# Performance work log

Measured on AMD Instinct MI355X. Metric: run time of the kernel, lower is better.

Reference implementation:

```python
import jax, jax.numpy as jnp
import numpy as np

D_MODEL = 1024
NHEAD = 16
HEAD_DIM = D_MODEL // NHEAD
B, T = 2, 2048


def setup_inputs() -> dict:
    key = jax.random.key(0)
    ks = jax.random.split(key, 12)
    s = 1.0 / np.sqrt(D_MODEL)
    return {
        "query": jax.random.normal(ks[0], (B, T, D_MODEL), jnp.float32),
        "key": jax.random.normal(ks[1], (B, T, D_MODEL), jnp.float32),
        "value": jax.random.normal(ks[2], (B, T, D_MODEL), jnp.float32),
        "key_padding_mask": jnp.zeros((B, T), dtype=bool),
        "attn_mask": jnp.zeros((T, T), jnp.float32),
        "stoich_frac": jax.random.uniform(ks[3], (B, T), jnp.float32),
        "Wq": jax.random.uniform(ks[4], (D_MODEL, D_MODEL), jnp.float32, -s, s),
        "bq": jnp.zeros((D_MODEL,), jnp.float32),
        "Wk": jax.random.uniform(ks[5], (D_MODEL, D_MODEL), jnp.float32, -s, s),
        "bk": jnp.zeros((D_MODEL,), jnp.float32),
        "Wv": jax.random.uniform(ks[6], (D_MODEL, D_MODEL), jnp.float32, -s, s),
        "bv": jnp.zeros((D_MODEL,), jnp.float32),
        "Wo": jax.random.uniform(ks[7], (D_MODEL, D_MODEL), jnp.float32, -s, s),
        "bo": jnp.zeros((D_MODEL,), jnp.float32),
        "stoich_alpha": jnp.float32(0.1),
    }


def reference(query, key, value, key_padding_mask, attn_mask, stoich_frac,
              Wq, bq, Wk, bk, Wv, bv, Wo, bo, stoich_alpha):
    Bq, Tq, _ = query.shape
    Tk = key.shape[1]
    scale = HEAD_DIM ** -0.5
    # Linear projections (torch Linear: x @ W.T + b), reshape to [B, H, T, Dh]
    Q = (query @ Wq.T + bq).reshape(Bq, Tq, NHEAD, HEAD_DIM).transpose(0, 2, 1, 3)
    K = (key @ Wk.T + bk).reshape(Bq, Tk, NHEAD, HEAD_DIM).transpose(0, 2, 1, 3)
    V = (value @ Wv.T + bv).reshape(Bq, Tk, NHEAD, HEAD_DIM).transpose(0, 2, 1, 3)
    # Scores [B, H, Tq, Tk]
    scores = jnp.einsum("bhqd,bhkd->bhqk", Q, K) * scale
    # Stoichiometric pairwise bias (T_q == T_k path)
    diff = stoich_frac[:, :, None] - stoich_frac[:, None, :]  # [B, Tq, Tk]
    bias = stoich_alpha * (jnp.log1p(jnp.abs(diff)) * jnp.sign(diff))
    scores = scores + bias[:, None, :, :]
    scores = scores + attn_mask  # broadcasts [Tq, Tk]
    scores = jnp.where(key_padding_mask[:, None, None, :], -jnp.inf, scores)
    probs = jax.nn.softmax(scores, axis=-1)
    # dropout: eval mode / p=0 -> identity
    out = jnp.einsum("bhqk,bhkd->bhqd", probs, V)
    out = out.transpose(0, 2, 1, 3).reshape(Bq, Tq, D_MODEL)
    return out @ Wo.T + bo
```

## Files before the change

### kernel.cpp

```cpp
#include <hip/hip_runtime.h>
#include <math.h>

typedef __bf16 bf16_t;
typedef __bf16 bf16x8 __attribute__((ext_vector_type(8)));
typedef __bf16 bf16x4 __attribute__((ext_vector_type(4)));
typedef float  f32x4  __attribute__((ext_vector_type(4)));

#define NHEAD 16
#define HDIM 64
#define DMODEL 1024
#define TSEQ 2048
#define WEL (DMODEL * DMODEL)

#define SBAR() __builtin_amdgcn_s_barrier()
#define SCHED0() __builtin_amdgcn_sched_barrier(0)
#define LGKM0() do { asm volatile("s_waitcnt lgkmcnt(0)" ::: "memory"); \
                     __builtin_amdgcn_sched_barrier(0); } while (0)

__device__ __forceinline__ f32x4 mfma16(bf16x8 a, bf16x8 b, f32x4 c) {
  return __builtin_amdgcn_mfma_f32_16x16x32_bf16(a, b, c, 0, 0, 0);
}

__device__ __forceinline__ void gload16(const bf16_t* g, bf16_t* l) {
  __builtin_amdgcn_global_load_lds((const __attribute__((address_space(1))) void*)g,
                                   (__attribute__((address_space(3))) void*)l, 16, 0, 0);
}

__device__ __forceinline__ unsigned pk2(float lo, float hi) {
  unsigned short a = __builtin_bit_cast(unsigned short, (__bf16)lo);
  unsigned short c = __builtin_bit_cast(unsigned short, (__bf16)hi);
  return ((unsigned)c << 16) | a;
}

__device__ __forceinline__ void cvtstore(f32x4 x0, f32x4 x1, bf16_t* dh, bf16_t* dl, int off) {
  bf16x8 hfr, lfr;
#pragma unroll
  for (int j = 0; j < 4; ++j) {
    float v = x0[j];
    __bf16 hb = (__bf16)v;
    hfr[j] = hb; lfr[j] = (__bf16)(v - (float)hb);
    float w = x1[j];
    __bf16 wb = (__bf16)w;
    hfr[4 + j] = wb; lfr[4 + j] = (__bf16)(w - (float)wb);
  }
  *(bf16x8*)(dh + off) = hfr;
  *(bf16x8*)(dl + off) = lfr;
}

__global__ __launch_bounds__(256)
void presplit_w(const float* __restrict__ w0, const float* __restrict__ w1,
                const float* __restrict__ w2, const float* __restrict__ w3,
                bf16_t* __restrict__ out) {
  const int y = blockIdx.y;
  const float* src = (y == 0) ? w0 : (y == 1) ? w1 : (y == 2) ? w2 : w3;
  size_t i = ((size_t)blockIdx.x * 256 + threadIdx.x) * 8;
  f32x4 a = *(const f32x4*)(src + i);
  f32x4 c = *(const f32x4*)(src + i + 4);
  bf16x8 h, l;
#pragma unroll
  for (int j = 0; j < 4; ++j) {
    __bf16 hb = (__bf16)a[j];
    h[j] = hb; l[j] = (__bf16)(a[j] - (float)hb);
    __bf16 cb = (__bf16)c[j];
    h[4 + j] = cb; l[4 + j] = (__bf16)(c[j] - (float)cb);
  }
  bf16_t* dh = out + (size_t)y * 2 * WEL;
  *(bf16x8*)(dh + i) = h;
  *(bf16x8*)(dh + WEL + i) = l;
}

__global__ __launch_bounds__(256)
void build_bias(const float* __restrict__ amask, const unsigned char* __restrict__ kpm,
                const float* __restrict__ sf, const float* __restrict__ alpha_p,
                bf16_t* __restrict__ BM) {
  size_t idx = (size_t)blockIdx.x * 256 + threadIdx.x;
  int k8 = (int)(idx & (TSEQ / 8 - 1));
  size_t bq = idx >> 8;
  int b = (int)(bq >> 11);
  int q = (int)(bq & (TSEQ - 1));
  const float sfq = sf[bq];
  const float alpha = *alpha_p;
  const float* sfk = sf + (size_t)b * TSEQ + k8 * 8;
  const float* am  = amask + (size_t)q * TSEQ + k8 * 8;
  const unsigned char* kp = kpm + (size_t)b * TSEQ + k8 * 8;
  bf16x8 o;
#pragma unroll
  for (int j = 0; j < 8; ++j) {
    float df = sfq - sfk[j];
    float v = alpha * copysignf(log1pf(fabsf(df)), df) + am[j];
    if (kp[j]) v = -1.0e30f;
    o[j] = (__bf16)v;
  }
  *(bf16x8*)&BM[idx * 8] = o;
}

template<int MODE>
__global__ __launch_bounds__(512)
void gemm_qkv(const float* __restrict__ A, const bf16_t* __restrict__ Wh,
              const bf16_t* __restrict__ Wl, const float* __restrict__ bias,
              bf16_t* __restrict__ obh, bf16_t* __restrict__ obl) {
  __shared__ bf16_t AH[8 * 512], AL[8 * 512], WHs[2][4 * 512], WLs[2][4 * 512];
  const int tid = threadIdx.x;
  const int lane = tid & 63;
  const int a15 = lane & 15, g = lane >> 4;
  const int wv = tid >> 6, wm = wv >> 1, wn = wv & 1;
  const int m0 = blockIdx.y * 128, n0 = blockIdx.x * 64;
  f32x4 acc[2][2] = {};

  const int t0 = tid >> 6, l0 = tid & 63;
  const float* pA = A + (size_t)(m0 + t0 * 16 + (l0 & 15)) * DMODEL + 8 * (l0 >> 4);
  const int wts = wv & 3;
  const bf16_t* pWg = ((wv < 4) ? Wh : Wl) + (size_t)(n0 + wts * 16 + a15) * DMODEL + 8 * g;

  f32x4 rAa = *(const f32x4*)pA, rAb = *(const f32x4*)(pA + 4);
  gload16(pWg, (wv < 4) ? &WHs[0][wts * 512] : &WLs[0][wts * 512]);

  constexpr int NK = DMODEL / 32;
  for (int t = 0; t < NK; ++t) {
    const int cur = t & 1;
    SBAR();
    cvtstore(rAa, rAb, AH, AL, tid * 8);
    SCHED0();
    if (t + 1 < NK) {
      pA += 32;
      rAa = *(const f32x4*)pA; rAb = *(const f32x4*)(pA + 4);
      SCHED0();
      gload16(pWg + (t + 1) * 32, (wv < 4) ? &WHs[cur ^ 1][wts * 512]
                                           : &WLs[cur ^ 1][wts * 512]);
      SCHED0();
      asm volatile("s_waitcnt vmcnt(3)" ::: "memory");
    } else {
      asm volatile("s_waitcnt vmcnt(0)" ::: "memory");
    }
    LGKM0();
    SBAR();

    bf16x8 ah[2], al[2], wh[2], wl[2];
#pragma unroll
    for (int i = 0; i < 2; ++i) {
      ah[i] = *(const bf16x8*)&AH[(wm * 2 + i) * 512 + lane * 8];
      al[i] = *(const bf16x8*)&AL[(wm * 2 + i) * 512 + lane * 8];
      wh[i] = *(const bf16x8*)&WHs[cur][(wn * 2 + i) * 512 + lane * 8];
      wl[i] = *(const bf16x8*)&WLs[cur][(wn * 2 + i) * 512 + lane * 8];
    }
    __builtin_amdgcn_s_setprio(1);
    if (MODE == 2) {
#pragma unroll
      for (int i = 0; i < 2; ++i)
#pragma unroll
        for (int j = 0; j < 2; ++j) {
          acc[i][j] = mfma16(wh[i], ah[j], acc[i][j]);
          acc[i][j] = mfma16(wh[i], al[j], acc[i][j]);
          acc[i][j] = mfma16(wl[i], ah[j], acc[i][j]);
        }
    } else {
#pragma unroll
      for (int i = 0; i < 2; ++i)
#pragma unroll
        for (int j = 0; j < 2; ++j) {
          acc[i][j] = mfma16(ah[i], wh[j], acc[i][j]);
          acc[i][j] = mfma16(ah[i], wl[j], acc[i][j]);
          acc[i][j] = mfma16(al[i], wh[j], acc[i][j]);
        }
    }
    __builtin_amdgcn_s_setprio(0);
  }

  if (MODE == 1) {
#pragma unroll
    for (int i = 0; i < 2; ++i)
#pragma unroll
      for (int j = 0; j < 2; ++j) {
        int n = n0 + wn * 32 + j * 16 + a15;
        float bs = bias[n];
        int hh = n >> 6, d = n & 63;
#pragma unroll
        for (int r = 0; r < 4; ++r) {
          int m = m0 + wm * 32 + i * 16 + 4 * g + r;
          int bb = m >> 11, t = m & (TSEQ - 1);
          float v = acc[i][j][r] + bs;
          size_t o = (((size_t)(bb * NHEAD + hh)) * TSEQ + t) * HDIM + d;
          __bf16 hb = (__bf16)v;
          obh[o] = hb;
          obl[o] = (__bf16)(v - (float)hb);
        }
      }
  } else {
#pragma unroll
    for (int i = 0; i < 2; ++i)
#pragma unroll
      for (int j = 0; j < 2; ++j) {
        int m = m0 + wm * 32 + j * 16 + a15;
        int bb = m >> 11, t = m & (TSEQ - 1);
#pragma unroll
        for (int r = 0; r < 4; ++r) {
          int n = n0 + wn * 32 + i * 16 + 4 * g + r;
          float v = acc[i][j][r] + bias[n];
          int hh = n >> 6, d = n & 63;
          size_t o = (((size_t)(bb * NHEAD + hh)) * HDIM + d) * TSEQ + t;
          __bf16 hb = (__bf16)v;
          obh[o] = hb;
          obl[o] = (__bf16)(v - (float)hb);
        }
      }
  }
}

__global__ __launch_bounds__(512)
void gemm_out(const bf16_t* __restrict__ Ah, const bf16_t* __restrict__ Al,
              const bf16_t* __restrict__ Wh, const bf16_t* __restrict__ Wl,
              const float* __restrict__ bias, float* __restrict__ of) {
  __shared__ bf16_t AHs[2][8 * 512], ALs[2][8 * 512], WHs[2][4 * 512], WLs[2][4 * 512];
  const int tid = threadIdx.x;
  const int lane = tid & 63;
  const int a15 = lane & 15, g = lane >> 4;
  const int wv = tid >> 6, wm = wv >> 1, wn = wv & 1;
  const int m0 = blockIdx.y * 128, n0 = blockIdx.x * 64;
  f32x4 acc[2][2] = {};

  const bf16_t* pAh = Ah + (size_t)(m0 + wv * 16 + a15) * DMODEL + 8 * g;
  const bf16_t* pAl = Al + (size_t)(m0 + wv * 16 + a15) * DMODEL + 8 * g;
  const int wts = wv & 3;
  const bf16_t* pWg = ((wv < 4) ? Wh : Wl) + (size_t)(n0 + wts * 16 + a15) * DMODEL + 8 * g;

  auto stage = [&](int t, int buf) {
    gload16(pAh + t * 32, &AHs[buf][wv * 512]);
    gload16(pAl + t * 32, &ALs[buf][wv * 512]);
    gload16(pWg + t * 32, (wv < 4) ? &WHs[buf][wts * 512] : &WLs[buf][wts * 512]);
  };
  stage(0, 0);

  constexpr int NK = DMODEL / 32;
  for (int t = 0; t < NK; ++t) {
    const int cur = t & 1;
    if (t + 1 < NK) {
      stage(t + 1, cur ^ 1);
      asm volatile("s_waitcnt vmcnt(3)" ::: "memory");
    } else {
      asm volatile("s_waitcnt vmcnt(0)" ::: "memory");
    }
    SCHED0();
    SBAR();

    bf16x8 ah[2], al[2], wh[2], wl[2];
#pragma unroll
    for (int i = 0; i < 2; ++i) {
      ah[i] = *(const bf16x8*)&AHs[cur][(wm * 2 + i) * 512 + lane * 8];
      al[i] = *(const bf16x8*)&ALs[cur][(wm * 2 + i) * 512 + lane * 8];
      wh[i] = *(const bf16x8*)&WHs[cur][(wn * 2 + i) * 512 + lane * 8];
      wl[i] = *(const bf16x8*)&WLs[cur][(wn * 2 + i) * 512 + lane * 8];
    }
    __builtin_amdgcn_s_setprio(1);
#pragma unroll
    for (int i = 0; i < 2; ++i)
#pragma unroll
      for (int j = 0; j < 2; ++j) {
        acc[i][j] = mfma16(ah[i], wh[j], acc[i][j]);
        acc[i][j] = mfma16(ah[i], wl[j], acc[i][j]);
        acc[i][j] = mfma16(al[i], wh[j], acc[i][j]);
      }
    __builtin_amdgcn_s_setprio(0);
    SBAR();
  }

#pragma unroll
  for (int i = 0; i < 2; ++i)
#pragma unroll
    for (int j = 0; j < 2; ++j) {
      int n = n0 + wn * 32 + j * 16 + a15;
      float bs = bias[n];
#pragma unroll
      for (int r = 0; r < 4; ++r) {
        int m = m0 + wm * 32 + i * 16 + 4 * g + r;
        of[(size_t)m * DMODEL + n] = acc[i][j][r] + bs;
      }
    }
}

__global__ __launch_bounds__(512)
void attn_mfma(const bf16_t* __restrict__ Qhi, const bf16_t* __restrict__ Qlo,
               const bf16_t* __restrict__ Khi, const bf16_t* __restrict__ Klo,
               const bf16_t* __restrict__ Vth, const bf16_t* __restrict__ Vtl,
               const bf16_t* __restrict__ BMt,
               bf16_t* __restrict__ Oh, bf16_t* __restrict__ Ol) {
  __shared__ bf16_t KH[2][8 * 512], KL[2][8 * 512], VH[2][8 * 512], VL[2][8 * 512];
  __shared__ bf16_t PS[8 * 512];
  const int tid = threadIdx.x;
  const int lane = tid & 63, wv = tid >> 6;
  const int a15 = lane & 15, g = lane >> 4;
  const int b = blockIdx.z, h = blockIdx.y, q0 = blockIdx.x * 128;
  const int bh = b * NHEAD + h;
  const int qg = q0 + wv * 16 + a15;
  constexpr int NT = TSEQ / 64;

  const bf16_t* Qh_b = Qhi + ((size_t)bh * TSEQ + qg) * HDIM;
  const bf16_t* Ql_b = Qlo + ((size_t)bh * TSEQ + qg) * HDIM;
  const bf16_t* Kh_b = Khi + (size_t)bh * TSEQ * HDIM;
  const bf16_t* Kl_b = Klo + (size_t)bh * TSEQ * HDIM;
  const bf16_t* Vh_b = Vth + (size_t)bh * HDIM * TSEQ;
  const bf16_t* Vl_b = Vtl + (size_t)bh * HDIM * TSEQ;
  const bf16_t* bmrow = BMt + ((size_t)b * TSEQ + qg) * TSEQ;

  bf16x8 qh[2], ql[2];
  qh[0] = *(const bf16x8*)&Qh_b[8 * g];
  qh[1] = *(const bf16x8*)&Qh_b[32 + 8 * g];
  ql[0] = *(const bf16x8*)&Ql_b[8 * g];
  ql[1] = *(const bf16x8*)&Ql_b[32 + 8 * g];

  f32x4 aco[4] = {};
  float m_run = -3.0e38f, l_run = 0.f;
  bf16x4 bmv[4], bmn[4];

  const int ts = wv >> 1, ks = wv & 1;
  auto stage = [&](int k0, int buf) {
    size_t ko = (size_t)(k0 + 16 * ts + a15) * HDIM + 32 * ks + 8 * g;
    gload16(Kh_b + ko, &KH[buf][wv * 512]);
    gload16(Kl_b + ko, &KL[buf][wv * 512]);
    size_t vo = (size_t)(16 * ts + a15) * TSEQ + k0 + 32 * ks + 8 * g;
    gload16(Vh_b + vo, &VH[buf][wv * 512]);
    gload16(Vl_b + vo, &VL[buf][wv * 512]);
  };

#pragma unroll
  for (int mt = 0; mt < 4; ++mt) bmv[mt] = *(const bf16x4*)&bmrow[16 * mt + 4 * g];
  stage(0, 0);

  const int psb = wv * 512 + a15 * 32;
  const int r3 = a15 & 3;

  for (int t = 0; t < NT; ++t) {
    const int cur = t & 1;
    if (t + 1 < NT) {
      const int kn = (t + 1) * 64;
#pragma unroll
      for (int mt = 0; mt < 4; ++mt) bmn[mt] = *(const bf16x4*)&bmrow[kn + 16 * mt + 4 * g];
      stage(kn, cur ^ 1);
      asm volatile("s_waitcnt vmcnt(8)" ::: "memory");
    } else {
      asm volatile("s_waitcnt vmcnt(0)" ::: "memory");
    }
    SCHED0();
    SBAR();

    f32x4 s4[4];
    __builtin_amdgcn_s_setprio(1);
#pragma unroll
    for (int mt = 0; mt < 4; ++mt) {
      bf16x8 k0h = *(const bf16x8*)&KH[cur][(mt * 2 + 0) * 512 + lane * 8];
      bf16x8 k1h = *(const bf16x8*)&KH[cur][(mt * 2 + 1) * 512 + lane * 8];
      bf16x8 k0l = *(const bf16x8*)&KL[cur][(mt * 2 + 0) * 512 + lane * 8];
      bf16x8 k1l = *(const bf16x8*)&KL[cur][(mt * 2 + 1) * 512 + lane * 8];
      f32x4 sa = {};
      sa = mfma16(k0h, qh[0], sa);
      sa = mfma16(k1h, qh[1], sa);
      sa = mfma16(k0h, ql[0], sa);
      sa = mfma16(k1h, ql[1], sa);
      sa = mfma16(k0l, qh[0], sa);
      sa = mfma16(k1l, qh[1], sa);
      s4[mt] = sa;
    }
    __builtin_amdgcn_s_setprio(0);

#pragma unroll
    for (int mt = 0; mt < 4; ++mt)
#pragma unroll
      for (int r = 0; r < 4; ++r)
        s4[mt][r] = fmaf(s4[mt][r], 0.125f, (float)bmv[mt][r]);

    float tmax = -3.0e38f;
#pragma unroll
    for (int mt = 0; mt < 4; ++mt)
#pragma unroll
      for (int r = 0; r < 4; ++r) tmax = fmaxf(tmax, s4[mt][r]);
    tmax = fmaxf(tmax, __shfl_xor(tmax, 16));
    tmax = fmaxf(tmax, __shfl_xor(tmax, 32));
    if (!__all(tmax - m_run <= 8.0f)) {
      float mnew = fmaxf(m_run, tmax);
      float corr = __expf(m_run - mnew);
      l_run *= corr;
#pragma unroll
      for (int dt = 0; dt < 4; ++dt) aco[dt] *= corr;
      m_run = mnew;
    }
    float psum = 0.f;
    unsigned pk01[4], pk23[4];
#pragma unroll
    for (int mt = 0; mt < 4; ++mt) {
      float p0 = __expf(s4[mt][0] - m_run);
      float p1 = __expf(s4[mt][1] - m_run);
      float p2 = __expf(s4[mt][2] - m_run);
      float p3 = __expf(s4[mt][3] - m_run);
      psum += (p0 + p1) + (p2 + p3);
      pk01[mt] = pk2(p0, p1);
      pk23[mt] = pk2(p2, p3);
    }
    psum += __shfl_xor(psum, 16);
    psum += __shfl_xor(psum, 32);
    l_run += psum;

    __builtin_amdgcn_s_setprio(1);
#pragma unroll
    for (int kss = 0; kss < 2; ++kss) {
#pragma unroll
      for (int mh = 0; mh < 2; ++mh) {
        int mt = kss * 2 + mh;
        int phys = ((mh << 1) | (g >> 1)) ^ r3;
        uint2 w2;
        w2.x = pk01[mt];
        w2.y = pk23[mt];
        *(uint2*)&PS[psb + phys * 8 + (g & 1) * 4] = w2;
      }
      LGKM0();
      bf16x8 pf = *(const bf16x8*)&PS[psb + ((g ^ r3) << 3)];
#pragma unroll
      for (int dt = 0; dt < 4; ++dt) {
        bf16x8 vh = *(const bf16x8*)&VH[cur][(dt * 2 + kss) * 512 + lane * 8];
        bf16x8 vl = *(const bf16x8*)&VL[cur][(dt * 2 + kss) * 512 + lane * 8];
        aco[dt] = mfma16(vh, pf, aco[dt]);
        aco[dt] = mfma16(vl, pf, aco[dt]);
      }
    }
    __builtin_amdgcn_s_setprio(0);

    if (t + 1 < NT) {
#pragma unroll
      for (int mt = 0; mt < 4; ++mt) bmv[mt] = bmn[mt];
    }
    SBAR();
  }

  float inv = 1.0f / l_run;
#pragma unroll
  for (int dt = 0; dt < 4; ++dt) {
    f32x4 o = aco[dt] * inv;
    bf16x4 oh, ol;
#pragma unroll
    for (int r = 0; r < 4; ++r) {
      __bf16 hb = (__bf16)o[r];
      oh[r] = hb;
      ol[r] = (__bf16)(o[r] - (float)hb);
    }
    size_t off = ((size_t)b * TSEQ + qg) * DMODEL + h * HDIM + dt * 16 + 4 * g;
    *(bf16x4*)&Oh[off] = oh;
    *(bf16x4*)&Ol[off] = ol;
  }
}

extern "C" void kernel_launch(void* const* d_in, const int* in_sizes, int n_in,
                              void* d_out, int out_size, void* d_ws, size_t ws_size,
                              hipStream_t stream) {
  const float* query = (const float*)d_in[0];
  const float* key = (const float*)d_in[1];
  const float* value = (const float*)d_in[2];
  const unsigned char* kpm = (const unsigned char*)d_in[3];
  const float* amask = (const float*)d_in[4];
  const float* sf = (const float*)d_in[5];
  const float* Wq = (const float*)d_in[6];
  const float* bq = (const float*)d_in[7];
  const float* Wk = (const float*)d_in[8];
  const float* bk = (const float*)d_in[9];
  const float* Wv = (const float*)d_in[10];
  const float* bv = (const float*)d_in[11];
  const float* Wo = (const float*)d_in[12];
  const float* bo = (const float*)d_in[13];
  const float* alpha = (const float*)d_in[14];
  float* out = (float*)d_out;

  const size_t NEL = (size_t)2 * NHEAD * TSEQ * HDIM;
  bf16_t* p = (bf16_t*)d_ws;
  bf16_t* Qh = p;
  bf16_t* Ql = p + NEL;
  bf16_t* Kh = p + 2 * NEL;
  bf16_t* Kl = p + 3 * NEL;
  bf16_t* Vh = p + 4 * NEL;
  bf16_t* Vl = p + 5 * NEL;
  bf16_t* Oh = p + 6 * NEL;
  bf16_t* Ol = p + 7 * NEL;
  bf16_t* BMt = p + 8 * NEL;
  bf16_t* wsp = p + 10 * NEL;
  bf16_t* wqh = wsp + 0 * WEL, *wql = wsp + 1 * WEL;
  bf16_t* wkh = wsp + 2 * WEL, *wkl = wsp + 3 * WEL;
  bf16_t* wvh = wsp + 4 * WEL, *wvl = wsp + 5 * WEL;
  bf16_t* woh = wsp + 6 * WEL, *wol = wsp + 7 * WEL;

  presplit_w<<<dim3(WEL / (256 * 8), 4), dim3(256), 0, stream>>>(Wq, Wk, Wv, Wo, wsp);
  build_bias<<<dim3(4096), dim3(256), 0, stream>>>(amask, kpm, sf, alpha, BMt);

  dim3 gg(16, 32), gb(512);
  gemm_qkv<1><<<gg, gb, 0, stream>>>(query, wqh, wql, bq, Qh, Ql);
  gemm_qkv<1><<<gg, gb, 0, stream>>>(key, wkh, wkl, bk, Kh, Kl);
  gemm_qkv<2><<<gg, gb, 0, stream>>>(value, wvh, wvl, bv, Vh, Vl);
  dim3 ga(TSEQ / 128, NHEAD, 2);
  attn_mfma<<<ga, gb, 0, stream>>>(Qh, Ql, Kh, Kl, Vh, Vl, BMt, Oh, Ol);
  gemm_out<<<gg, gb, 0, stream>>>(Oh, Ol, woh, wol, bo, out);
}
```

Measured before the change: 347.2 us.

## Split QKV weights in-kernel, stage epilogue through LDS, defer softmax row-sum shuffles

The separate pre-split pass over Wq/Wk/Wv is removed. The QKV GEMM now loads fp32 weights and converts them to hi/lo bf16 in registers, using a single LDS buffer. The QKV epilogue writes results into LDS first, then issues coalesced 16-byte global stores instead of scattered 2-byte stores. In attention, the cross-lane reduction of the softmax denominator moves out of the key loop to the end. The trade-offs are more global fp32 weight traffic per GEMM block (each block re-splits its tile) and loss of the double-buffered async weight loads.

```diff
diff --git a/kernel.cpp b/kernel.cpp
--- a/kernel.cpp
+++ b/kernel.cpp
@@ -48,14 +48,10 @@
 }
 
 __global__ __launch_bounds__(256)
-void presplit_w(const float* __restrict__ w0, const float* __restrict__ w1,
-                const float* __restrict__ w2, const float* __restrict__ w3,
-                bf16_t* __restrict__ out) {
-  const int y = blockIdx.y;
-  const float* src = (y == 0) ? w0 : (y == 1) ? w1 : (y == 2) ? w2 : w3;
+void presplit_wo(const float* __restrict__ w, bf16_t* __restrict__ oh, bf16_t* __restrict__ ol) {
   size_t i = ((size_t)blockIdx.x * 256 + threadIdx.x) * 8;
-  f32x4 a = *(const f32x4*)(src + i);
-  f32x4 c = *(const f32x4*)(src + i + 4);
+  f32x4 a = *(const f32x4*)(w + i);
+  f32x4 c = *(const f32x4*)(w + i + 4);
   bf16x8 h, l;
 #pragma unroll
   for (int j = 0; j < 4; ++j) {
@@ -64,9 +60,8 @@
     __bf16 cb = (__bf16)c[j];
     h[4 + j] = cb; l[4 + j] = (__bf16)(c[j] - (float)cb);
   }
-  bf16_t* dh = out + (size_t)y * 2 * WEL;
-  *(bf16x8*)(dh + i) = h;
-  *(bf16x8*)(dh + WEL + i) = l;
+  *(bf16x8*)(oh + i) = h;
+  *(bf16x8*)(ol + i) = l;
 }
 
 __global__ __launch_bounds__(256)
@@ -96,10 +91,14 @@
 
 template<int MODE>
 __global__ __launch_bounds__(512)
-void gemm_qkv(const float* __restrict__ A, const bf16_t* __restrict__ Wh,
-              const bf16_t* __restrict__ Wl, const float* __restrict__ bias,
+void gemm_qkv(const float* __restrict__ A, const float* __restrict__ W,
+              const float* __restrict__ bias,
               bf16_t* __restrict__ obh, bf16_t* __restrict__ obl) {
-  __shared__ bf16_t AH[8 * 512], AL[8 * 512], WHs[2][4 * 512], WLs[2][4 * 512];
+  __shared__ bf16_t SM[12 * 1024];
+  bf16_t* AH = SM;
+  bf16_t* AL = SM + 4096;
+  bf16_t* WH = SM + 8192;
+  bf16_t* WL = SM + 10240;
   const int tid = threadIdx.x;
   const int lane = tid & 63;
   const int a15 = lane & 15, g = lane >> 4;
@@ -107,30 +106,26 @@
   const int m0 = blockIdx.y * 128, n0 = blockIdx.x * 64;
   f32x4 acc[2][2] = {};
 
-  const int t0 = tid >> 6, l0 = tid & 63;
-  const float* pA = A + (size_t)(m0 + t0 * 16 + (l0 & 15)) * DMODEL + 8 * (l0 >> 4);
-  const int wts = wv & 3;
-  const bf16_t* pWg = ((wv < 4) ? Wh : Wl) + (size_t)(n0 + wts * 16 + a15) * DMODEL + 8 * g;
+  const int st = tid >> 6, sl = tid & 63;
+  const float* pA = A + (size_t)(m0 + st * 16 + (sl & 15)) * DMODEL + 8 * (sl >> 4);
+  const bool doW = (tid < 256);
+  const int sW = tid & 255;
+  const int tw = sW >> 6, lw = sW & 63;
+  const float* pW = W + (size_t)(n0 + tw * 16 + (lw & 15)) * DMODEL + 8 * (lw >> 4);
 
   f32x4 rAa = *(const f32x4*)pA, rAb = *(const f32x4*)(pA + 4);
-  gload16(pWg, (wv < 4) ? &WHs[0][wts * 512] : &WLs[0][wts * 512]);
-
-  constexpr int NK = DMODEL / 32;
-  for (int t = 0; t < NK; ++t) {
-    const int cur = t & 1;
+  f32x4 rWa = {}, rWb = {};
+  if (doW) { rWa = *(const f32x4*)pW; rWb = *(const f32x4*)(pW + 4); }
+
+  for (int k0 = 0; k0 < DMODEL; k0 += 32) {
     SBAR();
     cvtstore(rAa, rAb, AH, AL, tid * 8);
+    if (doW) cvtstore(rWa, rWb, WH, WL, sW * 8);
     SCHED0();
-    if (t + 1 < NK) {
+    if (k0 + 32 < DMODEL) {
       pA += 32;
       rAa = *(const f32x4*)pA; rAb = *(const f32x4*)(pA + 4);
-      SCHED0();
-      gload16(pWg + (t + 1) * 32, (wv < 4) ? &WHs[cur ^ 1][wts * 512]
-                                           : &WLs[cur ^ 1][wts * 512]);
-      SCHED0();
-      asm volatile("s_waitcnt vmcnt(3)" ::: "memory");
-    } else {
-      asm volatile("s_waitcnt vmcnt(0)" ::: "memory");
+      if (doW) { pW += 32; rWa = *(const f32x4*)pW; rWb = *(const f32x4*)(pW + 4); }
     }
     LGKM0();
     SBAR();
@@ -140,11 +135,11 @@
     for (int i = 0; i < 2; ++i) {
       ah[i] = *(const bf16x8*)&AH[(wm * 2 + i) * 512 + lane * 8];
       al[i] = *(const bf16x8*)&AL[(wm * 2 + i) * 512 + lane * 8];
-      wh[i] = *(const bf16x8*)&WHs[cur][(wn * 2 + i) * 512 + lane * 8];
-      wl[i] = *(const bf16x8*)&WLs[cur][(wn * 2 + i) * 512 + lane * 8];
+      wh[i] = *(const bf16x8*)&WH[(wn * 2 + i) * 512 + lane * 8];
+      wl[i] = *(const bf16x8*)&WL[(wn * 2 + i) * 512 + lane * 8];
     }
     __builtin_amdgcn_s_setprio(1);
-    if (MODE == 2) {
+    if constexpr (MODE == 2) {
 #pragma unroll
       for (int i = 0; i < 2; ++i)
 #pragma unroll
@@ -166,43 +161,61 @@
     __builtin_amdgcn_s_setprio(0);
   }
 
-  if (MODE == 1) {
-#pragma unroll
-    for (int i = 0; i < 2; ++i)
-#pragma unroll
-      for (int j = 0; j < 2; ++j) {
-        int n = n0 + wn * 32 + j * 16 + a15;
-        float bs = bias[n];
-        int hh = n >> 6, d = n & 63;
-#pragma unroll
-        for (int r = 0; r < 4; ++r) {
-          int m = m0 + wm * 32 + i * 16 + 4 * g + r;
-          int bb = m >> 11, t = m & (TSEQ - 1);
-          float v = acc[i][j][r] + bs;
-          size_t o = (((size_t)(bb * NHEAD + hh)) * TSEQ + t) * HDIM + d;
-          __bf16 hb = (__bf16)v;
-          obh[o] = hb;
-          obl[o] = (__bf16)(v - (float)hb);
+  const int hh = blockIdx.x;
+  const int bb2 = m0 >> 11;
+  const int tt0 = m0 & (TSEQ - 1);
+#pragma unroll
+  for (int pass = 0; pass < 2; ++pass) {
+    SBAR();
+    if constexpr (MODE == 1) {
+#pragma unroll
+      for (int i = 0; i < 2; ++i)
+#pragma unroll
+        for (int j = 0; j < 2; ++j) {
+          int d = wn * 32 + j * 16 + a15;
+          float bs = bias[hh * 64 + d];
+          int tl = wm * 32 + i * 16 + 4 * g;
+#pragma unroll
+          for (int r = 0; r < 4; ++r) {
+            float v = acc[i][j][r] + bs;
+            __bf16 hb = (__bf16)v;
+            SM[(tl + r) * 64 + d] = (pass == 0) ? hb : (__bf16)(v - (float)hb);
+          }
         }
+    } else {
+#pragma unroll
+      for (int i = 0; i < 2; ++i)
+#pragma unroll
+        for (int j = 0; j < 2; ++j) {
+          int tl = wm * 32 + j * 16 + a15;
+#pragma unroll
+          for (int r = 0; r < 4; ++r) {
+            int d = wn * 32 + i * 16 + 4 * g + r;
+            float v = acc[i][j][r] + bias[hh * 64 + d];
+            __bf16 hb = (__bf16)v;
+            SM[d * 128 + tl] = (pass == 0) ? hb : (__bf16)(v - (float)hb);
+          }
+        }
+    }
+    LGKM0();
+    SBAR();
+    bf16_t* dst = (pass == 0) ? obh : obl;
+    if constexpr (MODE == 1) {
+      size_t gbase = (((size_t)(bb2 * NHEAD + hh)) * TSEQ + tt0) * HDIM;
+#pragma unroll
+      for (int pp = 0; pp < 2; ++pp) {
+        int idx = pp * 4096 + tid * 8;
+        *(uint4*)(dst + gbase + idx) = *(const uint4*)&SM[idx];
       }
-  } else {
-#pragma unroll
-    for (int i = 0; i < 2; ++i)
-#pragma unroll
-      for (int j = 0; j < 2; ++j) {
-        int m = m0 + wm * 32 + j * 16 + a15;
-        int bb = m >> 11, t = m & (TSEQ - 1);
-#pragma unroll
-        for (int r = 0; r < 4; ++r) {
-          int n = n0 + wn * 32 + i * 16 + 4 * g + r;
-          float v = acc[i][j][r] + bias[n];
-          int hh = n >> 6, d = n & 63;
-          size_t o = (((size_t)(bb * NHEAD + hh)) * HDIM + d) * TSEQ + t;
-          __bf16 hb = (__bf16)v;
-          obh[o] = hb;
-          obl[o] = (__bf16)(v - (float)hb);
-        }
+    } else {
+      size_t vb = ((size_t)(bb2 * NHEAD + hh)) * HDIM * TSEQ;
+#pragma unroll
+      for (int pp = 0; pp < 2; ++pp) {
+        int idx = pp * 4096 + tid * 8;
+        int dd = idx >> 7, tt = idx & 127;
+        *(uint4*)(dst + vb + (size_t)dd * TSEQ + tt0 + tt) = *(const uint4*)&SM[idx];
       }
+    }
   }
 }
 
@@ -394,8 +407,6 @@
       pk01[mt] = pk2(p0, p1);
       pk23[mt] = pk2(p2, p3);
     }
-    psum += __shfl_xor(psum, 16);
-    psum += __shfl_xor(psum, 32);
     l_run += psum;
 
     __builtin_amdgcn_s_setprio(1);
@@ -428,6 +439,9 @@
     }
     SBAR();
   }
+
+  l_run += __shfl_xor(l_run, 16);
+  l_run += __shfl_xor(l_run, 32);
 
   float inv = 1.0f / l_run;
 #pragma unroll
@@ -477,20 +491,19 @@
   bf16_t* Oh = p + 6 * NEL;
   bf16_t* Ol = p + 7 * NEL;
   bf16_t* BMt = p + 8 * NEL;
-  bf16_t* wsp = p + 10 * NEL;
-  bf16_t* wqh = wsp + 0 * WEL, *wql = wsp + 1 * WEL;
-  bf16_t* wkh = wsp + 2 * WEL, *wkl = wsp + 3 * WEL;
-  bf16_t* wvh = wsp + 4 * WEL, *wvl = wsp + 5 * WEL;
-  bf16_t* woh = wsp + 6 * WEL, *wol = wsp + 7 * WEL;
-
-  presplit_w<<<dim3(WEL / (256 * 8), 4), dim3(256), 0, stream>>>(Wq, Wk, Wv, Wo, wsp);
+  bf16_t* woh = p + 10 * NEL;
+  bf16_t* wol = p + 10 * NEL + WEL;
+
+  presplit_wo<<<dim3(WEL / (256 * 8)), dim3(256), 0, stream>>>(Wo, woh, wol);
   build_bias<<<dim3(4096), dim3(256), 0, stream>>>(amask, kpm, sf, alpha, BMt);
 
   dim3 gg(16, 32), gb(512);
-  gemm_qkv<1><<<gg, gb, 0, stream>>>(query, wqh, wql, bq, Qh, Ql);
-  gemm_qkv<1><<<gg, gb, 0, stream>>>(key, wkh, wkl, bk, Kh, Kl);
-  gemm_qkv<2><<<gg, gb, 0, stream>>>(value, wvh, wvl, bv, Vh, Vl);
+  gemm_qkv<1><<<gg, gb, 0, stream>>>(query, Wq, bq, Qh, Ql);
+  gemm_qkv<1><<<gg, gb, 0, stream>>>(key, Wk, bk, Kh, Kl);
+  gemm_qkv<2><<<gg, gb, 0, stream>>>(value, Wv, bv, Vh, Vl);
+
   dim3 ga(TSEQ / 128, NHEAD, 2);
   attn_mfma<<<ga, gb, 0, stream>>>(Qh, Ql, Kh, Kl, Vh, Vl, BMt, Oh, Ol);
+
   gemm_out<<<gg, gb, 0, stream>>>(Oh, Ol, woh, wol, bo, out);
 }
```

Result: no change. 344.7 us (-0.7%).
